# Kernel tuning notes

Measured on AMD Instinct MI355X. Metric: run time of the kernel, lower is better.

The kernel has to match this reference:

```python
import jax, jax.numpy as jnp
import numpy as np

B, T, C = 2, 2048, 1024
N_HEAD = 16
HEAD = C // N_HEAD


def setup_inputs() -> dict:
    key = jax.random.key(0)
    k1, k2, k3 = jax.random.split(key, 3)
    x = jax.random.normal(k1, (B, T, C), dtype=jnp.float32)
    w_qkv = jax.random.normal(k2, (3 * C, C), dtype=jnp.float32) * 0.02
    w_proj = jax.random.normal(k3, (C, C), dtype=jnp.float32) * 0.02
    return {"x": x, "w_qkv": w_qkv, "w_proj": w_proj}


def reference(x, w_qkv, w_proj):
    b, t, c = x.shape
    # c_attn: y = x @ W^T  (no bias). Split rows of W into q/k/v blocks.
    wq, wk, wv = jnp.split(w_qkv, 3, axis=0)            # each [C, C]
    q = (x @ wq.T).reshape(b, t, N_HEAD, HEAD)          # [B,T,H,D]
    k = (x @ wk.T).reshape(b, t, N_HEAD, HEAD)
    v = (x @ wv.T).reshape(b, t, N_HEAD, HEAD)
    scale = 1.0 / np.sqrt(HEAD).astype(np.float32)
    scores = jnp.einsum('bqhd,bkhd->bhqk', q, k) * scale  # [B,H,T,T]
    causal = jnp.tril(jnp.ones((t, t), dtype=bool))
    scores = jnp.where(causal, scores, -jnp.inf)
    attn = jax.nn.softmax(scores, axis=-1)               # [B,H,T,T]
    out = jnp.einsum('bhqk,bkhd->bqhd', attn, v).reshape(b, t, c)
    return out @ w_proj.T
```

## Files before the change

### kernel.cpp

```cpp
#include <hip/hip_runtime.h>
#include <hip/hip_bf16.h>


typedef __attribute__((ext_vector_type(8))) short bf16x8;
typedef __attribute__((ext_vector_type(4))) short bf16x4;
typedef __attribute__((ext_vector_type(4))) float floatx4;
typedef __attribute__((ext_vector_type(16))) float f32x16;

#define MFMA16(a, b, c) __builtin_amdgcn_mfma_f32_16x16x32_bf16((a), (b), (c), 0, 0, 0)
#define MFMA32(a, b, c) __builtin_amdgcn_mfma_f32_32x32x16_bf16((a), (b), (c), 0, 0, 0)

#if __has_builtin(__builtin_amdgcn_exp2f)
#define EXP2F(x) __builtin_amdgcn_exp2f(x)
#else
#define EXP2F(x) exp2f(x)
#endif

static constexpr int Bc = 2, Tc = 2048, Cc = 1024, Hc = 16, Dc = 64;
static constexpr size_t QKV_STRIDE = (size_t)Bc * Hc * Tc * Dc;
static constexpr float KSL2E = 0.125f * 1.44269504088896f;

__device__ __forceinline__ bf16x8 load8(const __hip_bfloat16* p) {
    return *(const bf16x8*)p;
}

__device__ __forceinline__ short f2b(float x) {
    union { __hip_bfloat16 h; short s; } u;
    u.h = __float2bfloat16(x);
    return u.s;
}

__device__ __forceinline__ bf16x8 pack8(floatx4 a, floatx4 b) {
    bf16x8 r;
    r[0] = f2b(a[0]); r[1] = f2b(a[1]); r[2] = f2b(a[2]); r[3] = f2b(a[3]);
    r[4] = f2b(b[0]); r[5] = f2b(b[1]); r[6] = f2b(b[2]); r[7] = f2b(b[3]);
    return r;
}

__device__ __forceinline__ unsigned pk2(float a, float b) {
    return (unsigned)(unsigned short)f2b(a) |
           ((unsigned)(unsigned short)f2b(b) << 16);
}

__device__ __forceinline__ void pl32swap(unsigned& a, unsigned& b) {
    asm volatile("v_permlane32_swap_b32 %0, %1" : "+v"(a), "+v"(b));
}

__device__ __forceinline__ bf16x8 mk8(unsigned a, unsigned b, unsigned c, unsigned d) {
    union { unsigned u[4]; bf16x8 v; } x;
    x.u[0] = a; x.u[1] = b; x.u[2] = c; x.u[3] = d;
    return x.v;
}

__device__ __forceinline__ void gl2lds16(const void* g, void* l) {
    __builtin_amdgcn_global_load_lds(
        (const __attribute__((address_space(1))) void*)g,
        (__attribute__((address_space(3))) void*)l, 16, 0, 0);
}

__global__ __launch_bounds__(256) void cvt_bf16(
    const float* __restrict__ in, __hip_bfloat16* __restrict__ out, int n8) {
    const int i = blockIdx.x * 256 + threadIdx.x;
    if (i < n8) {
        const floatx4 a = *(const floatx4*)&in[(size_t)i * 8];
        const floatx4 b = *(const floatx4*)&in[(size_t)i * 8 + 4];
        *(bf16x8*)&out[(size_t)i * 8] = pack8(a, b);
    }
}

__global__ __launch_bounds__(256) void gemm_qkv_bf16(
    const __hip_bfloat16* __restrict__ A,
    const __hip_bfloat16* __restrict__ W,
    __hip_bfloat16* __restrict__ qkv) {
    __shared__ __hip_bfloat16 As16[128 * 32];
    __shared__ __hip_bfloat16 Bs16[128 * 32];
    const int K = Cc;
    const int lane = threadIdx.x & 63;
    const int wave = threadIdx.x >> 6;
    const int waveM = wave >> 1, waveN = wave & 1;
    const int mBase = blockIdx.x * 128;
    const int nBase = blockIdx.y * 128;
    const int idx16 = lane & 15;
    const int quad = lane >> 4;
    const int aRow = lane >> 2, aPos = lane & 3;

    floatx4 acc[4][4] = {};

    for (int k0 = 0; k0 < K; k0 += 32) {
        __syncthreads();
#pragma unroll
        for (int s = 0; s < 2; s++) {
            const int r0 = wave * 32 + s * 16;
            const int row = r0 + aRow;
            const int cg = aPos ^ (row & 3);
            gl2lds16(A + (size_t)(mBase + row) * K + k0 + cg * 8, &As16[r0 * 32]);
            gl2lds16(W + (size_t)(nBase + row) * K + k0 + cg * 8, &Bs16[r0 * 32]);
        }
        __syncthreads();

        bf16x8 af[4], bfr[4];
#pragma unroll
        for (int i = 0; i < 4; i++) {
            const int rr = waveM * 64 + i * 16 + idx16;
            af[i] = *(const bf16x8*)&As16[rr * 32 + ((quad ^ (rr & 3)) * 8)];
        }
#pragma unroll
        for (int j = 0; j < 4; j++) {
            const int rr = waveN * 64 + j * 16 + idx16;
            bfr[j] = *(const bf16x8*)&Bs16[rr * 32 + ((quad ^ (rr & 3)) * 8)];
        }
#pragma unroll
        for (int i = 0; i < 4; i++)
#pragma unroll
            for (int j = 0; j < 4; j++)
                acc[i][j] = MFMA16(af[i], bfr[j], acc[i][j]);
    }

#pragma unroll
    for (int i = 0; i < 4; i++) {
#pragma unroll
        for (int j = 0; j < 4; j++) {
            const int n = nBase + waveN * 64 + j * 16 + idx16;
            const int part = n >> 10;
            const int rem = n & 1023;
            const int h = rem >> 6, d = rem & 63;
#pragma unroll
            for (int r = 0; r < 4; r++) {
                const int m = mBase + waveM * 64 + i * 16 + quad * 4 + r;
                const int bb = m >> 11, t = m & 2047;
                const size_t o = (size_t)part * QKV_STRIDE +
                                 (((size_t)(bb * Hc + h)) * Tc + t) * Dc + d;
                qkv[o] = __float2bfloat16(acc[i][j][r]);
            }
        }
    }
}

__global__ __launch_bounds__(256) void gemm_proj_bf16(
    const __hip_bfloat16* __restrict__ A,
    const __hip_bfloat16* __restrict__ W,
    float* __restrict__ out) {
    __shared__ __hip_bfloat16 As16[128 * 32];
    __shared__ __hip_bfloat16 Bs16[128 * 32];
    const int K = Cc;
    const int lane = threadIdx.x & 63;
    const int wave = threadIdx.x >> 6;
    const int waveM = wave >> 1, waveN = wave & 1;
    const int mBase = blockIdx.x * 128;
    const int nBase = blockIdx.y * 128;
    const int idx16 = lane & 15;
    const int quad = lane >> 4;
    const int aRow = lane >> 2, aPos = lane & 3;

    floatx4 acc[4][4] = {};

    for (int k0 = 0; k0 < K; k0 += 32) {
        __syncthreads();
#pragma unroll
        for (int s = 0; s < 2; s++) {
            const int r0 = wave * 32 + s * 16;
            const int row = r0 + aRow;
            const int cg = aPos ^ (row & 3);
            gl2lds16(A + (size_t)(mBase + row) * K + k0 + cg * 8, &As16[r0 * 32]);
            gl2lds16(W + (size_t)(nBase + row) * K + k0 + cg * 8, &Bs16[r0 * 32]);
        }
        __syncthreads();

        bf16x8 af[4], bfr[4];
#pragma unroll
        for (int i = 0; i < 4; i++) {
            const int rr = waveM * 64 + i * 16 + idx16;
            af[i] = *(const bf16x8*)&As16[rr * 32 + ((quad ^ (rr & 3)) * 8)];
        }
#pragma unroll
        for (int j = 0; j < 4; j++) {
            const int rr = waveN * 64 + j * 16 + idx16;
            bfr[j] = *(const bf16x8*)&Bs16[rr * 32 + ((quad ^ (rr & 3)) * 8)];
        }
#pragma unroll
        for (int i = 0; i < 4; i++)
#pragma unroll
            for (int j = 0; j < 4; j++)
                acc[i][j] = MFMA16(af[i], bfr[j], acc[i][j]);
    }

#pragma unroll
    for (int i = 0; i < 4; i++) {
#pragma unroll
        for (int j = 0; j < 4; j++) {
            const int n = nBase + waveN * 64 + j * 16 + idx16;
#pragma unroll
            for (int r = 0; r < 4; r++) {
                const int m = mBase + waveM * 64 + i * 16 + quad * 4 + r;
                out[(size_t)m * Cc + n] = acc[i][j][r];
            }
        }
    }
}

__global__ __launch_bounds__(256) void transpose_v(
    const __hip_bfloat16* __restrict__ v,
    __hip_bfloat16* __restrict__ vt) {
    __shared__ unsigned short tile[64][65];
    const int t0 = blockIdx.x * 64;
    const int h = blockIdx.y, b = blockIdx.z;
    const size_t base = ((size_t)(b * Hc + h)) * Tc * Dc;
    const unsigned short* vp = (const unsigned short*)v + base;
    unsigned short* vtp = (unsigned short*)vt + base;

    for (int e = threadIdx.x; e < 4096; e += 256) {
        const int tl = e >> 6, d = e & 63;
        tile[tl][d] = vp[(size_t)(t0 + tl) * Dc + d];
    }
    __syncthreads();
    for (int e = threadIdx.x; e < 4096; e += 256) {
        const int d = e >> 6, tl = e & 63;
        vtp[(size_t)d * Tc + t0 + tl] = tile[tl][d];
    }
}

__global__ __launch_bounds__(512) void attn_fold(
    const __hip_bfloat16* __restrict__ qkv,
    const __hip_bfloat16* __restrict__ vt,
    __hip_bfloat16* __restrict__ aout) {
    __shared__ floatx4 smem4[4096];
    char* const smem = (char*)smem4;
    __hip_bfloat16* const kA = (__hip_bfloat16*)smem;
    __hip_bfloat16* const vA = kA + 8192;
    __hip_bfloat16* const kB = vA + 8192;
    __hip_bfloat16* const vB = kB + 8192;
    float* const comb = (float*)smem;

    const int lane = threadIdx.x & 63;
    const int wave = threadIdx.x >> 6;
    const int c31 = lane & 31;
    const int hw = lane >> 5;
    const int p = blockIdx.x;
    const int h = blockIdx.y;
    const int b = blockIdx.z;
    const int H = 15 - p, L = p;
    const int lightEnd = 2 * p + 2;
    const int w3 = wave & 3;

    const size_t headOff = ((size_t)(b * Hc + h)) * Tc * Dc;
    const __hip_bfloat16* qp = qkv + headOff;
    const __hip_bfloat16* kp = qkv + QKV_STRIDE + headOff;
    const __hip_bfloat16* vtp = vt + headOff;

    int qB = ((wave < 4) ? H : L) * 128 + w3 * 32;
    int qtw = (qB + 31) >> 6;
    int qMax = qB + 31;
    int qg = qB + c31;

    bf16x8 qf0, qf1, qf2, qf3;
    auto loadQ = [&]() {
        const __hip_bfloat16* qr = qp + (size_t)qg * Dc + hw * 8;
        qf0 = load8(qr);
        qf1 = load8(qr + 16);
        qf2 = load8(qr + 32);
        qf3 = load8(qr + 48);
    };
    loadQ();

    f32x16 O0 = {}, O1 = {};
    float lacc = 0.f;

    auto stageA = [&](int kt, int buf) {
        const int keyBase = kt * 64;
#pragma unroll
        for (int s = 0; s < 2; s++) {
            const int blk = w3 * 2 + s;
            const int row = blk * 8 + (lane >> 3);
            const int g = (lane & 7) ^ (row & 7);
            gl2lds16(kp + (size_t)(keyBase + row) * Dc + g * 8,
                     kA + buf * 4096 + blk * 512);
            gl2lds16(vtp + (size_t)row * Tc + keyBase + g * 8,
                     vA + buf * 4096 + blk * 512);
        }
    };
    auto stageB = [&](int kt, int buf) {
        const int keyBase = kt * 64;
#pragma unroll
        for (int s = 0; s < 2; s++) {
            const int blk = w3 * 2 + s;
            const int row = blk * 8 + (lane >> 3);
            const int g = (lane & 7) ^ (row & 7);
            gl2lds16(kp + (size_t)(keyBase + row) * Dc + g * 8,
                     kB + buf * 4096 + blk * 512);
            gl2lds16(vtp + (size_t)row * Tc + keyBase + g * 8,
                     vB + buf * 4096 + blk * 512);
        }
    };

    auto computeTile = [&](const __hip_bfloat16* kS, const __hip_bfloat16* vS,
                           int keyBase) {
#pragma unroll
        for (int kb = 0; kb < 2; kb++) {
            if (keyBase + kb * 32 <= qMax) {
                const int kr = kb * 32 + c31;
                const int m8 = kr & 7;
                f32x16 S = {};
                S = MFMA32(load8(&kS[kr * 64 + (((0 + hw) ^ m8) * 8)]), qf0, S);
                S = MFMA32(load8(&kS[kr * 64 + (((2 + hw) ^ m8) * 8)]), qf1, S);
                S = MFMA32(load8(&kS[kr * 64 + (((4 + hw) ^ m8) * 8)]), qf2, S);
                S = MFMA32(load8(&kS[kr * 64 + (((6 + hw) ^ m8) * 8)]), qf3, S);

                unsigned w[8];
#pragma unroll
                for (int r = 0; r < 16; r += 2) {
                    const int key0 = keyBase + kb * 32 +
                                     (r & 3) + 8 * (r >> 2) + 4 * hw;
                    float p0 = EXP2F(S[r] * KSL2E);
                    p0 = (key0 > qg) ? 0.f : p0;
                    float p1 = EXP2F(S[r + 1] * KSL2E);
                    p1 = (key0 + 1 > qg) ? 0.f : p1;
                    lacc += p0 + p1;
                    w[r >> 1] = pk2(p0, p1);
                }
                pl32swap(w[0], w[2]);
                pl32swap(w[1], w[3]);
                pl32swap(w[4], w[6]);
                pl32swap(w[5], w[7]);
                const bf16x8 pA0 = mk8(w[0], w[1], w[2], w[3]);
                const bf16x8 pA1 = mk8(w[4], w[5], w[6], w[7]);

                {
                    const int vr = c31;
                    const int vm = vr & 7;
                    const bf16x8 vf0 = load8(&vS[vr * 64 + (((kb * 4 + hw) ^ vm) * 8)]);
                    const bf16x8 vf1 = load8(&vS[vr * 64 + (((kb * 4 + 2 + hw) ^ vm) * 8)]);
                    O0 = MFMA32(pA0, vf0, O0);
                    O0 = MFMA32(pA1, vf1, O0);
                }
                {
                    const int vr = 32 + c31;
                    const int vm = vr & 7;
                    const bf16x8 vf0 = load8(&vS[vr * 64 + (((kb * 4 + hw) ^ vm) * 8)]);
                    const bf16x8 vf1 = load8(&vS[vr * 64 + (((kb * 4 + 2 + hw) ^ vm) * 8)]);
                    O1 = MFMA32(pA0, vf0, O1);
                    O1 = MFMA32(pA1, vf1, O1);
                }
            }
        }
    };

    auto outStore = [&](int qB_, float ltot) {
#pragma unroll
        for (int r = 0; r < 16; r++) {
            const int qrl = (r & 3) + 8 * (r >> 2) + 4 * hw;
            const float lr = __shfl(ltot, qrl, 64);
            const float inv = 1.0f / lr;
            const size_t rowOff = ((size_t)(b * Tc + qB_ + qrl)) * Cc + h * 64;
            aout[rowOff + c31] = __float2bfloat16(O0[r] * inv);
            aout[rowOff + 32 + c31] = __float2bfloat16(O1[r] * inv);
        }
    };

    if (wave < 4) stageA(0, 0);

    for (int i = 0; i < 17; i++) {
        __syncthreads();
        if (i < 16) {
            if (wave < 4) stageA(i + 1, (i + 1) & 1);
            else if (i + 1 >= lightEnd) stageB(i + 16 - 2 * p, (i + 1) & 1);
        }
        if (wave >= 4 && i == lightEnd) {
            outStore(qB, lacc + __shfl_xor(lacc, 32, 64));
#pragma unroll
            for (int r = 0; r < 16; r++) { O0[r] = 0.f; O1[r] = 0.f; }
            lacc = 0.f;
            qB = H * 128 + w3 * 32;
            qtw = (qB + 31) >> 6;
            qMax = qB + 31;
            qg = qB + c31;
            loadQ();
        }
        if (wave < 4) {
            computeTile(kA + (i & 1) * 4096, vA + (i & 1) * 4096, i * 64);
        } else if (i < lightEnd) {
            if (i <= qtw)
                computeTile(kA + (i & 1) * 4096, vA + (i & 1) * 4096, i * 64);
        } else {
            const int kt = i + 15 - 2 * p;
            if (kt <= qtw)
                computeTile(kB + (i & 1) * 4096, vB + (i & 1) * 4096, kt * 64);
        }
        __syncthreads();
    }

    const float ltotOwn = lacc + __shfl_xor(lacc, 32, 64);
    if (wave >= 4) {
        float* c = comb + (size_t)(wave - 4) * 2112;
#pragma unroll
        for (int r = 0; r < 16; r++) {
            c[r * 64 + lane] = O0[r];
            c[(16 + r) * 64 + lane] = O1[r];
        }
        c[2048 + lane] = ltotOwn;
    }
    __syncthreads();
    if (wave < 4) {
        float* c = comb + (size_t)wave * 2112;
#pragma unroll
        for (int r = 0; r < 16; r++) {
            O0[r] += c[r * 64 + lane];
            O1[r] += c[(16 + r) * 64 + lane];
        }
        outStore(qB, ltotOwn + c[2048 + lane]);
    }
}

__global__ __launch_bounds__(256) void gemm_qkv(
    const float* __restrict__ A,
    const float* __restrict__ W,
    __hip_bfloat16* __restrict__ qkv) {
    __shared__ float As[128 * 32];
    __shared__ float Bs[128 * 32];
    const int K = Cc;
    const int lane = threadIdx.x & 63;
    const int wave = threadIdx.x >> 6;
    const int waveM = wave >> 1, waveN = wave & 1;
    const int mBase = blockIdx.x * 128;
    const int nBase = blockIdx.y * 128;
    const int idx16 = lane & 15;
    const int quad = lane >> 4;
    const int ldRow = lane >> 3;
    const int ldPos = lane & 7;

    floatx4 acc[4][4] = {};

    for (int k0 = 0; k0 < K; k0 += 32) {
        __syncthreads();
#pragma unroll
        for (int s = 0; s < 4; s++) {
            const int r0 = wave * 32 + s * 8;
            const int row = r0 + ldRow;
            const int cg = ldPos ^ (row & 7);
            gl2lds16(A + (size_t)(mBase + row) * K + k0 + cg * 4, &As[r0 * 32]);
            gl2lds16(W + (size_t)(nBase + row) * K + k0 + cg * 4, &Bs[r0 * 32]);
        }
        __syncthreads();

        bf16x8 af[4], bfr[4];
#pragma unroll
        for (int i = 0; i < 4; i++) {
            const int rr = waveM * 64 + i * 16 + idx16;
            const floatx4 a0 = *(const floatx4*)&As[rr * 32 + (((quad * 2) ^ (rr & 7)) * 4)];
            const floatx4 a1 = *(const floatx4*)&As[rr * 32 + (((quad * 2 + 1) ^ (rr & 7)) * 4)];
            af[i] = pack8(a0, a1);
        }
#pragma unroll
        for (int j = 0; j < 4; j++) {
            const int rr = waveN * 64 + j * 16 + idx16;
            const floatx4 b0 = *(const floatx4*)&Bs[rr * 32 + (((quad * 2) ^ (rr & 7)) * 4)];
            const floatx4 b1 = *(const floatx4*)&Bs[rr * 32 + (((quad * 2 + 1) ^ (rr & 7)) * 4)];
            bfr[j] = pack8(b0, b1);
        }
#pragma unroll
        for (int i = 0; i < 4; i++)
#pragma unroll
            for (int j = 0; j < 4; j++)
                acc[i][j] = MFMA16(af[i], bfr[j], acc[i][j]);
    }

#pragma unroll
    for (int i = 0; i < 4; i++) {
#pragma unroll
        for (int j = 0; j < 4; j++) {
            const int n = nBase + waveN * 64 + j * 16 + idx16;
            const int part = n >> 10;
            const int rem = n & 1023;
            const int h = rem >> 6, d = rem & 63;
#pragma unroll
            for (int r = 0; r < 4; r++) {
                const int m = mBase + waveM * 64 + i * 16 + quad * 4 + r;
                const int bb = m >> 11, t = m & 2047;
                const size_t o = (size_t)part * QKV_STRIDE +
                                 (((size_t)(bb * Hc + h)) * Tc + t) * Dc + d;
                qkv[o] = __float2bfloat16(acc[i][j][r]);
            }
        }
    }
}

__global__ __launch_bounds__(256) void gemm_proj(
    const __hip_bfloat16* __restrict__ A,
    const float* __restrict__ W,
    float* __restrict__ out) {
    __shared__ __hip_bfloat16 As16[128 * 32];
    __shared__ float Ws[64 * 32];
    const int K = Cc;
    const int lane = threadIdx.x & 63;
    const int wave = threadIdx.x >> 6;
    const int waveM = wave >> 1, waveN = wave & 1;
    const int mBase = blockIdx.x * 128;
    const int nBase = blockIdx.y * 64;
    const int idx16 = lane & 15;
    const int quad = lane >> 4;
    const int aRow = lane >> 2, aPos = lane & 3;
    const int wRow = lane >> 3, wPos = lane & 7;

    floatx4 acc[4][2] = {};

    for (int k0 = 0; k0 < K; k0 += 32) {
        __syncthreads();
#pragma unroll
        for (int s = 0; s < 2; s++) {
            {
                const int r0 = wave * 32 + s * 16;
                const int row = r0 + aRow;
                const int cg = aPos ^ (row & 3);
                gl2lds16(A + (size_t)(mBase + row) * K + k0 + cg * 8, &As16[r0 * 32]);
            }
            {
                const int r0 = wave * 16 + s * 8;
                const int row = r0 + wRow;
                const int cg = wPos ^ (row & 7);
                gl2lds16(W + (size_t)(nBase + row) * K + k0 + cg * 4, &Ws[r0 * 32]);
            }
        }
        __syncthreads();

        bf16x8 af[4], bfr[2];
#pragma unroll
        for (int i = 0; i < 4; i++) {
            const int rr = waveM * 64 + i * 16 + idx16;
            af[i] = *(const bf16x8*)&As16[rr * 32 + ((quad ^ (rr & 3)) * 8)];
        }
#pragma unroll
        for (int j = 0; j < 2; j++) {
            const int rr = waveN * 32 + j * 16 + idx16;
            const floatx4 b0 = *(const floatx4*)&Ws[rr * 32 + (((quad * 2) ^ (rr & 7)) * 4)];
            const floatx4 b1 = *(const floatx4*)&Ws[rr * 32 + (((quad * 2 + 1) ^ (rr & 7)) * 4)];
            bfr[j] = pack8(b0, b1);
        }
#pragma unroll
        for (int i = 0; i < 4; i++)
#pragma unroll
            for (int j = 0; j < 2; j++)
                acc[i][j] = MFMA16(af[i], bfr[j], acc[i][j]);
    }

#pragma unroll
    for (int i = 0; i < 4; i++) {
#pragma unroll
        for (int j = 0; j < 2; j++) {
            const int n = nBase + waveN * 32 + j * 16 + idx16;
#pragma unroll
            for (int r = 0; r < 4; r++) {
                const int m = mBase + waveM * 64 + i * 16 + quad * 4 + r;
                out[(size_t)m * Cc + n] = acc[i][j][r];
            }
        }
    }
}

extern "C" void kernel_launch(void* const* d_in, const int* in_sizes, int n_in,
                              void* d_out, int out_size, void* d_ws, size_t ws_size,
                              hipStream_t stream) {
    const float* x = nullptr;
    const float* w_qkv = nullptr;
    const float* w_proj = nullptr;
    for (int i = 0; i < n_in; i++) {
        if (in_sizes[i] == 4194304) x = (const float*)d_in[i];
        else if (in_sizes[i] == 3145728) w_qkv = (const float*)d_in[i];
        else if (in_sizes[i] == 1048576) w_proj = (const float*)d_in[i];
    }
    float* out = (float*)d_out;

    __hip_bfloat16* qkv = (__hip_bfloat16*)d_ws;
    __hip_bfloat16* vbuf = qkv + 2 * QKV_STRIDE;
    __hip_bfloat16* vt = qkv + 3 * QKV_STRIDE;
    __hip_bfloat16* ao = vbuf;

    const size_t CVT_OFF = 8 * QKV_STRIDE;
    const size_t NEED = CVT_OFF + (4194304 + 3145728) * sizeof(__hip_bfloat16);

    if (ws_size >= NEED) {
        __hip_bfloat16* xb = (__hip_bfloat16*)((char*)d_ws + CVT_OFF);
        __hip_bfloat16* wbq = xb + 4194304;
        __hip_bfloat16* wbp = qkv;

        cvt_bf16<<<dim3(4194304 / 8 / 256), 256, 0, stream>>>(x, xb, 4194304 / 8);
        cvt_bf16<<<dim3(3145728 / 8 / 256), 256, 0, stream>>>(w_qkv, wbq, 3145728 / 8);
        gemm_qkv_bf16<<<dim3(4096 / 128, 3072 / 128), 256, 0, stream>>>(xb, wbq, qkv);
        transpose_v<<<dim3(Tc / 64, Hc, Bc), 256, 0, stream>>>(vbuf, vt);
        attn_fold<<<dim3(8, Hc, Bc), 512, 0, stream>>>(qkv, vt, ao);
        cvt_bf16<<<dim3(1048576 / 8 / 256), 256, 0, stream>>>(w_proj, wbp, 1048576 / 8);
        gemm_proj_bf16<<<dim3(4096 / 128, 1024 / 128), 256, 0, stream>>>(ao, wbp, out);
    } else {
        gemm_qkv<<<dim3(4096 / 128, 3072 / 128), 256, 0, stream>>>(x, w_qkv, qkv);
        transpose_v<<<dim3(Tc / 64, Hc, Bc), 256, 0, stream>>>(vbuf, vt);
        attn_fold<<<dim3(8, Hc, Bc), 512, 0, stream>>>(qkv, vt, ao);
        gemm_proj<<<dim3(4096 / 128, 1024 / 64), 256, 0, stream>>>(ao, w_proj, out);
    }
}
```

Measured before the change: 188.0 us.

## Swizzle QKV GEMM blocks, shrink proj tile, skip unneeded causal masks, drop barrier

The QKV GEMM remaps block indices so consecutive blocks spread across tiles, aiming for better cache locality across chiplets. The projection GEMM uses 128x64 tiles, doubling the block count to fill more CUs. The attention kernel adds a mask-free path for key tiles fully below the diagonal and removes the per-iteration trailing barrier, relying on the leading barrier for double-buffer safety. Fewer sync points add some race risk, and smaller proj tiles reduce operand reuse.

```diff
diff --git a/kernel.cpp b/kernel.cpp
--- a/kernel.cpp
+++ b/kernel.cpp
@@ -78,8 +78,10 @@
     const int lane = threadIdx.x & 63;
     const int wave = threadIdx.x >> 6;
     const int waveM = wave >> 1, waveN = wave & 1;
-    const int mBase = blockIdx.x * 128;
-    const int nBase = blockIdx.y * 128;
+    const int flat = blockIdx.y * 32 + blockIdx.x;
+    const int swz = (flat & 7) * 96 + (flat >> 3);
+    const int mBase = (swz & 31) * 128;
+    const int nBase = (swz >> 5) * 128;
     const int idx16 = lane & 15;
     const int quad = lane >> 4;
     const int aRow = lane >> 2, aPos = lane & 3;
@@ -141,18 +143,18 @@
     const __hip_bfloat16* __restrict__ W,
     float* __restrict__ out) {
     __shared__ __hip_bfloat16 As16[128 * 32];
-    __shared__ __hip_bfloat16 Bs16[128 * 32];
+    __shared__ __hip_bfloat16 Bs16[64 * 32];
     const int K = Cc;
     const int lane = threadIdx.x & 63;
     const int wave = threadIdx.x >> 6;
     const int waveM = wave >> 1, waveN = wave & 1;
     const int mBase = blockIdx.x * 128;
-    const int nBase = blockIdx.y * 128;
+    const int nBase = blockIdx.y * 64;
     const int idx16 = lane & 15;
     const int quad = lane >> 4;
     const int aRow = lane >> 2, aPos = lane & 3;
 
-    floatx4 acc[4][4] = {};
+    floatx4 acc[4][2] = {};
 
     for (int k0 = 0; k0 < K; k0 += 32) {
         __syncthreads();
@@ -162,33 +164,38 @@
             const int row = r0 + aRow;
             const int cg = aPos ^ (row & 3);
             gl2lds16(A + (size_t)(mBase + row) * K + k0 + cg * 8, &As16[r0 * 32]);
+        }
+        {
+            const int r0 = wave * 16;
+            const int row = r0 + aRow;
+            const int cg = aPos ^ (row & 3);
             gl2lds16(W + (size_t)(nBase + row) * K + k0 + cg * 8, &Bs16[r0 * 32]);
         }
         __syncthreads();
 
-        bf16x8 af[4], bfr[4];
+        bf16x8 af[4], bfr[2];
 #pragma unroll
         for (int i = 0; i < 4; i++) {
             const int rr = waveM * 64 + i * 16 + idx16;
             af[i] = *(const bf16x8*)&As16[rr * 32 + ((quad ^ (rr & 3)) * 8)];
         }
 #pragma unroll
-        for (int j = 0; j < 4; j++) {
-            const int rr = waveN * 64 + j * 16 + idx16;
+        for (int j = 0; j < 2; j++) {
+            const int rr = waveN * 32 + j * 16 + idx16;
             bfr[j] = *(const bf16x8*)&Bs16[rr * 32 + ((quad ^ (rr & 3)) * 8)];
         }
 #pragma unroll
         for (int i = 0; i < 4; i++)
 #pragma unroll
-            for (int j = 0; j < 4; j++)
+            for (int j = 0; j < 2; j++)
                 acc[i][j] = MFMA16(af[i], bfr[j], acc[i][j]);
     }
 
 #pragma unroll
     for (int i = 0; i < 4; i++) {
 #pragma unroll
-        for (int j = 0; j < 4; j++) {
-            const int n = nBase + waveN * 64 + j * 16 + idx16;
+        for (int j = 0; j < 2; j++) {
+            const int n = nBase + waveN * 32 + j * 16 + idx16;
 #pragma unroll
             for (int r = 0; r < 4; r++) {
                 const int m = mBase + waveM * 64 + i * 16 + quad * 4 + r;
@@ -293,7 +300,7 @@
     };
 
     auto computeTile = [&](const __hip_bfloat16* kS, const __hip_bfloat16* vS,
-                           int keyBase) {
+                           int keyBase, bool msk) {
 #pragma unroll
         for (int kb = 0; kb < 2; kb++) {
             if (keyBase + kb * 32 <= qMax) {
@@ -306,16 +313,26 @@
                 S = MFMA32(load8(&kS[kr * 64 + (((6 + hw) ^ m8) * 8)]), qf3, S);
 
                 unsigned w[8];
-#pragma unroll
-                for (int r = 0; r < 16; r += 2) {
-                    const int key0 = keyBase + kb * 32 +
-                                     (r & 3) + 8 * (r >> 2) + 4 * hw;
-                    float p0 = EXP2F(S[r] * KSL2E);
-                    p0 = (key0 > qg) ? 0.f : p0;
-                    float p1 = EXP2F(S[r + 1] * KSL2E);
-                    p1 = (key0 + 1 > qg) ? 0.f : p1;
-                    lacc += p0 + p1;
-                    w[r >> 1] = pk2(p0, p1);
+                if (msk) {
+#pragma unroll
+                    for (int r = 0; r < 16; r += 2) {
+                        const int key0 = keyBase + kb * 32 +
+                                         (r & 3) + 8 * (r >> 2) + 4 * hw;
+                        float p0 = EXP2F(S[r] * KSL2E);
+                        p0 = (key0 > qg) ? 0.f : p0;
+                        float p1 = EXP2F(S[r + 1] * KSL2E);
+                        p1 = (key0 + 1 > qg) ? 0.f : p1;
+                        lacc += p0 + p1;
+                        w[r >> 1] = pk2(p0, p1);
+                    }
+                } else {
+#pragma unroll
+                    for (int r = 0; r < 16; r += 2) {
+                        const float p0 = EXP2F(S[r] * KSL2E);
+                        const float p1 = EXP2F(S[r + 1] * KSL2E);
+                        lacc += p0 + p1;
+                        w[r >> 1] = pk2(p0, p1);
+                    }
                 }
                 pl32swap(w[0], w[2]);
                 pl32swap(w[1], w[3]);
@@ -376,17 +393,20 @@
             loadQ();
         }
         if (wave < 4) {
-            computeTile(kA + (i & 1) * 4096, vA + (i & 1) * 4096, i * 64);
+            computeTile(kA + (i & 1) * 4096, vA + (i & 1) * 4096, i * 64,
+                        i * 64 + 63 > qB);
         } else if (i < lightEnd) {
             if (i <= qtw)
-                computeTile(kA + (i & 1) * 4096, vA + (i & 1) * 4096, i * 64);
+                computeTile(kA + (i & 1) * 4096, vA + (i & 1) * 4096, i * 64,
+                            i * 64 + 63 > qB);
         } else {
             const int kt = i + 15 - 2 * p;
             if (kt <= qtw)
-                computeTile(kB + (i & 1) * 4096, vB + (i & 1) * 4096, kt * 64);
-        }
-        __syncthreads();
-    }
+                computeTile(kB + (i & 1) * 4096, vB + (i & 1) * 4096, kt * 64,
+                            kt * 64 + 63 > qB);
+        }
+    }
+    __syncthreads();
 
     const float ltotOwn = lacc + __shfl_xor(lacc, 32, 64);
     if (wave >= 4) {
@@ -587,7 +607,7 @@
         transpose_v<<<dim3(Tc / 64, Hc, Bc), 256, 0, stream>>>(vbuf, vt);
         attn_fold<<<dim3(8, Hc, Bc), 512, 0, stream>>>(qkv, vt, ao);
         cvt_bf16<<<dim3(1048576 / 8 / 256), 256, 0, stream>>>(w_proj, wbp, 1048576 / 8);
-        gemm_proj_bf16<<<dim3(4096 / 128, 1024 / 128), 256, 0, stream>>>(ao, wbp, out);
+        gemm_proj_bf16<<<dim3(4096 / 128, 1024 / 64), 256, 0, stream>>>(ao, wbp, out);
     } else {
         gemm_qkv<<<dim3(4096 / 128, 3072 / 128), 256, 0, stream>>>(x, w_qkv, qkv);
         transpose_v<<<dim3(Tc / 64, Hc, Bc), 256, 0, stream>>>(vbuf, vt);
```

Measured after the change: 181.1 us. 1.04x faster.
